# Kernel tuning notes

Measured on AMD Instinct MI355X. Metric: run time of the kernel, lower is better.

## Reference

```python
import jax, jax.numpy as jnp
import numpy as np


def setup_inputs() -> dict:
    key = jax.random.key(0)
    k1, k2 = jax.random.split(key)
    B, T, S, D = 8, 1024, 1024, 2048
    support_sets = jax.random.normal(k1, (B, S, D), dtype=jnp.float32)
    X_hats = jax.random.normal(k2, (B, T, D), dtype=jnp.float32)
    return {"support_sets": support_sets, "X_hats": X_hats}


def reference(support_sets, X_hats):
    # Pairwise cosine similarity: out[b, t, s] = cos(X_hats[b, t], support_sets[b, s])
    # Matches torch.nn.functional.cosine_similarity with eps=1e-10:
    #   dot / max(||x|| * ||y||, eps)
    eps = 1e-10
    x_norm = jnp.linalg.norm(X_hats, axis=-1)          # [B, T]
    s_norm = jnp.linalg.norm(support_sets, axis=-1)    # [B, S]
    dots = jnp.einsum('btd,bsd->bts', X_hats, support_sets)  # [B, T, S]
    denom = jnp.maximum(x_norm[:, :, None] * s_norm[:, None, :], eps)
    return dots / denom
```

## Files before the change

kernel.cpp:

```cpp
#include <hip/hip_runtime.h>
#include <hip/hip_bf16.h>

typedef __attribute__((ext_vector_type(4))) float        f32x4;
typedef __attribute__((ext_vector_type(8))) short        s16x8;
typedef __attribute__((ext_vector_type(4))) unsigned int u32x4;
typedef __attribute__((ext_vector_type(2))) unsigned int u32x2;

#define Bb 8
#define Tt 1024
#define Ss 1024
#define Dd 2048
#define BM 128
#define BN 128
#define BK 64

__device__ __forceinline__ unsigned pack2_bf16(float f0, float f1) {
  unsigned u0 = __builtin_bit_cast(unsigned, f0) + 0x8000u;
  unsigned u1 = __builtin_bit_cast(unsigned, f1) + 0x8000u;
  return (u0 >> 16) | (u1 & 0xffff0000u);
}

__device__ __forceinline__ void gld_lds16(const void* g, void* l) {
  __builtin_amdgcn_global_load_lds(
      (__attribute__((address_space(1))) void*)(void*)(g),
      (__attribute__((address_space(3))) void*)l, 16, 0, 0);
}

__global__ __launch_bounds__(256, 4)
void convert_kernel(const float* __restrict__ sup, const float* __restrict__ xh,
                    unsigned* __restrict__ abf, unsigned* __restrict__ bbf,
                    float* __restrict__ invA, float* __restrict__ invB)
{
  const int wave = threadIdx.x >> 6, lane = threadIdx.x & 63;
  const int rowg = (blockIdx.x * 4 + wave) * 2;
  const float* src; unsigned* dst; float* inv; int row;
  if (rowg < 8192) { row = rowg;         src = xh;  dst = abf; inv = invA; }
  else             { row = rowg - 8192;  src = sup; dst = bbf; inv = invB; }

  const f32x4* s0 = (const f32x4*)(src + (size_t)row * Dd);
  const f32x4* s1 = (const f32x4*)(src + (size_t)(row + 1) * Dd);
  u32x2* d0 = (u32x2*)(dst + (size_t)row * (Dd / 2));
  u32x2* d1 = (u32x2*)(dst + (size_t)(row + 1) * (Dd / 2));
  float sq0 = 0.0f, sq1 = 0.0f;
  #pragma unroll
  for (int j = 0; j < 8; ++j) {
    f32x4 v0 = s0[j * 64 + lane];
    f32x4 v1 = s1[j * 64 + lane];
    sq0 = fmaf(v0[0], v0[0], fmaf(v0[1], v0[1], fmaf(v0[2], v0[2], fmaf(v0[3], v0[3], sq0))));
    sq1 = fmaf(v1[0], v1[0], fmaf(v1[1], v1[1], fmaf(v1[2], v1[2], fmaf(v1[3], v1[3], sq1))));
    d0[j * 64 + lane] = (u32x2){pack2_bf16(v0[0], v0[1]), pack2_bf16(v0[2], v0[3])};
    d1[j * 64 + lane] = (u32x2){pack2_bf16(v1[0], v1[1]), pack2_bf16(v1[2], v1[3])};
  }
  #pragma unroll
  for (int m = 32; m; m >>= 1) { sq0 += __shfl_xor(sq0, m, 64); sq1 += __shfl_xor(sq1, m, 64); }
  if (lane == 0) { inv[row] = 1.0f / sqrtf(sq0); inv[row + 1] = 1.0f / sqrtf(sq1); }
}

__global__ __launch_bounds__(256, 2)
void gemm_kernel(const short* __restrict__ abf, const short* __restrict__ bbf,
                 const float* __restrict__ invA, const float* __restrict__ invB,
                 float* __restrict__ out)
{
  __shared__ short As[BM * BK];
  __shared__ short Bs[BN * BK];

  const int bid  = blockIdx.x;
  const int b    = bid >> 6;
  const int tile = bid & 63;
  const int tm   = tile >> 3;
  const int tn   = tile & 7;

  const int t = threadIdx.x, wave = t >> 6, lane = t & 63;

  const int srow = lane >> 3;
  const int cph  = lane & 7;
  const int r0   = wave * 32;

  const size_t aRow = (size_t)(b * Tt + tm * BM);
  const size_t bRow = (size_t)(b * Ss + tn * BN);
  const short *gA0, *gA1, *gA2, *gA3, *gB0, *gB1, *gB2, *gB3;
  {
    int r;
    r = r0 + 0 * 8 + srow; gA0 = abf + (aRow + r) * Dd + (cph ^ (r & 7)) * 8;
                           gB0 = bbf + (bRow + r) * Dd + (cph ^ (r & 7)) * 8;
    r = r0 + 1 * 8 + srow; gA1 = abf + (aRow + r) * Dd + (cph ^ (r & 7)) * 8;
                           gB1 = bbf + (bRow + r) * Dd + (cph ^ (r & 7)) * 8;
    r = r0 + 2 * 8 + srow; gA2 = abf + (aRow + r) * Dd + (cph ^ (r & 7)) * 8;
                           gB2 = bbf + (bRow + r) * Dd + (cph ^ (r & 7)) * 8;
    r = r0 + 3 * 8 + srow; gA3 = abf + (aRow + r) * Dd + (cph ^ (r & 7)) * 8;
                           gB3 = bbf + (bRow + r) * Dd + (cph ^ (r & 7)) * 8;
  }
  short* lA0 = As + (r0 + 0)  * BK;
  short* lA1 = As + (r0 + 8)  * BK;
  short* lA2 = As + (r0 + 16) * BK;
  short* lA3 = As + (r0 + 24) * BK;
  short* lB0 = Bs + (r0 + 0)  * BK;
  short* lB1 = Bs + (r0 + 8)  * BK;
  short* lB2 = Bs + (r0 + 16) * BK;
  short* lB3 = Bs + (r0 + 24) * BK;

  const int wm = (wave >> 1) << 6;
  const int wn = (wave & 1) << 6;
  const int lm = lane & 15;
  const int kq = lane >> 4;

  f32x4 acc[4][4];
  #pragma unroll
  for (int i = 0; i < 4; ++i)
    #pragma unroll
    for (int j = 0; j < 4; ++j)
      acc[i][j] = (f32x4)0.0f;

  for (int k0 = 0; k0 < Dd; k0 += BK) {
    __syncthreads();
    gld_lds16(gA0, lA0); gld_lds16(gA1, lA1); gld_lds16(gA2, lA2); gld_lds16(gA3, lA3);
    gld_lds16(gB0, lB0); gld_lds16(gB1, lB1); gld_lds16(gB2, lB2); gld_lds16(gB3, lB3);
    gA0 += BK; gA1 += BK; gA2 += BK; gA3 += BK;
    gB0 += BK; gB1 += BK; gB2 += BK; gB3 += BK;
    __syncthreads();

    #pragma unroll
    for (int ks = 0; ks < 2; ++ks) {
      const int pchunk = ((ks * 4 + kq) ^ (lm & 7)) * 8;
      s16x8 af[4], bfr[4];
      #pragma unroll
      for (int i = 0; i < 4; ++i) {
        af[i]  = *(const s16x8*)(As + (wm + i * 16 + lm) * BK + pchunk);
        bfr[i] = *(const s16x8*)(Bs + (wn + i * 16 + lm) * BK + pchunk);
      }
      #pragma unroll
      for (int mi = 0; mi < 4; ++mi)
        #pragma unroll
        for (int ni = 0; ni < 4; ++ni)
          acc[mi][ni] = __builtin_amdgcn_mfma_f32_16x16x32_bf16(af[mi], bfr[ni], acc[mi][ni], 0, 0, 0);
    }
  }

  const float* iA = invA + b * Tt + tm * BM;
  const float* iB = invB + b * Ss + tn * BN;
  float* outb = out + (size_t)(b * Tt + tm * BM) * Ss + tn * BN;
  const int m0 = wm + kq * 4;
  const int n0 = wn + lm;
  #pragma unroll
  for (int mi = 0; mi < 4; ++mi) {
    #pragma unroll
    for (int r = 0; r < 4; ++r) {
      const int mrow = m0 + mi * 16 + r;
      const float ia = iA[mrow];
      float* orow = outb + (size_t)mrow * Ss;
      #pragma unroll
      for (int ni = 0; ni < 4; ++ni) {
        const int ncol = n0 + ni * 16;
        orow[ncol] = acc[mi][ni][r] * (ia * iB[ncol]);
      }
    }
  }
}

#define LDKF 40
#define BKF 32
__global__ __launch_bounds__(256, 2)
void paircos_kernel(const float* __restrict__ sup, const float* __restrict__ xh,
                    float* __restrict__ out)
{
  __shared__ short As[BM * LDKF];
  __shared__ short Bs[BN * LDKF];
  __shared__ float invA[BM];
  __shared__ float invB[BN];

  const int bid = blockIdx.x;
  const int b = bid >> 6, tile = bid & 63, tm = tile >> 3, tn = tile & 7;
  const float* Abase = xh  + (size_t)(b * Tt + tm * BM) * Dd;
  const float* Bbase = sup + (size_t)(b * Ss + tn * BN) * Dd;
  const int t = threadIdx.x, row = t >> 1, kh = t & 1;
  const f32x4* agp = (const f32x4*)(Abase + (size_t)row * Dd + kh * 16);
  const f32x4* bgp = (const f32x4*)(Bbase + (size_t)row * Dd + kh * 16);
  u32x4* awr = (u32x4*)(As + row * LDKF + kh * 16);
  u32x4* bwr = (u32x4*)(Bs + row * LDKF + kh * 16);
  const int wave = t >> 6, lane = t & 63;
  const int wm = (wave >> 1) << 6, wn = (wave & 1) << 6;
  const int lm = lane & 15, kq = lane >> 4;

  f32x4 acc[4][4];
  #pragma unroll
  for (int i = 0; i < 4; ++i)
    #pragma unroll
    for (int j = 0; j < 4; ++j) acc[i][j] = (f32x4)0.0f;
  float sqa = 0.0f, sqb = 0.0f;
  f32x4 areg[4], breg[4];
  #pragma unroll
  for (int i = 0; i < 4; ++i) { areg[i] = agp[i]; breg[i] = bgp[i]; }

  for (int k0 = 0; k0 < Dd; k0 += BKF) {
    unsigned pa[8], pb[8];
    #pragma unroll
    for (int i = 0; i < 4; ++i) {
      sqa = fmaf(areg[i][0], areg[i][0], sqa); sqa = fmaf(areg[i][1], areg[i][1], sqa);
      sqa = fmaf(areg[i][2], areg[i][2], sqa); sqa = fmaf(areg[i][3], areg[i][3], sqa);
      pa[i*2+0] = pack2_bf16(areg[i][0], areg[i][1]); pa[i*2+1] = pack2_bf16(areg[i][2], areg[i][3]);
      sqb = fmaf(breg[i][0], breg[i][0], sqb); sqb = fmaf(breg[i][1], breg[i][1], sqb);
      sqb = fmaf(breg[i][2], breg[i][2], sqb); sqb = fmaf(breg[i][3], breg[i][3], sqb);
      pb[i*2+0] = pack2_bf16(breg[i][0], breg[i][1]); pb[i*2+1] = pack2_bf16(breg[i][2], breg[i][3]);
    }
    __syncthreads();
    awr[0] = (u32x4){pa[0],pa[1],pa[2],pa[3]}; awr[1] = (u32x4){pa[4],pa[5],pa[6],pa[7]};
    bwr[0] = (u32x4){pb[0],pb[1],pb[2],pb[3]}; bwr[1] = (u32x4){pb[4],pb[5],pb[6],pb[7]};
    __syncthreads();
    if (k0 + BKF < Dd) {
      const int off = (k0 + BKF) >> 2;
      #pragma unroll
      for (int i = 0; i < 4; ++i) { areg[i] = agp[off + i]; breg[i] = bgp[off + i]; }
    }
    s16x8 af[4], bfr[4];
    #pragma unroll
    for (int i = 0; i < 4; ++i) {
      af[i]  = *(const s16x8*)(As + (wm + i*16 + lm) * LDKF + kq * 8);
      bfr[i] = *(const s16x8*)(Bs + (wn + i*16 + lm) * LDKF + kq * 8);
    }
    #pragma unroll
    for (int mi = 0; mi < 4; ++mi)
      #pragma unroll
      for (int ni = 0; ni < 4; ++ni)
        acc[mi][ni] = __builtin_amdgcn_mfma_f32_16x16x32_bf16(af[mi], bfr[ni], acc[mi][ni], 0, 0, 0);
  }
  __syncthreads();
  ((float*)As)[t] = sqa; ((float*)Bs)[t] = sqb;
  __syncthreads();
  if (t < 128) {
    invA[t] = 1.0f / sqrtf(((float*)As)[2*t] + ((float*)As)[2*t+1]);
    invB[t] = 1.0f / sqrtf(((float*)Bs)[2*t] + ((float*)Bs)[2*t+1]);
  }
  __syncthreads();
  float* outb = out + (size_t)(b * Tt + tm * BM) * Ss + tn * BN;
  const int m0 = wm + kq * 4, n0 = wn + lm;
  #pragma unroll
  for (int mi = 0; mi < 4; ++mi) {
    #pragma unroll
    for (int r = 0; r < 4; ++r) {
      const int mrow = m0 + mi * 16 + r;
      const float ia = invA[mrow];
      float* orow = outb + (size_t)mrow * Ss;
      #pragma unroll
      for (int ni = 0; ni < 4; ++ni) {
        const int ncol = n0 + ni * 16;
        orow[ncol] = acc[mi][ni][r] * (ia * invB[ncol]);
      }
    }
  }
}

extern "C" void kernel_launch(void* const* d_in, const int* in_sizes, int n_in,
                              void* d_out, int out_size, void* d_ws, size_t ws_size,
                              hipStream_t stream) {
  const float* sup = (const float*)d_in[0];
  const float* xh  = (const float*)d_in[1];
  float* out = (float*)d_out;

  const size_t nElem = (size_t)Bb * Tt * Dd;
  const size_t bfBytes = nElem * sizeof(short);
  const size_t NEED = 2 * bfBytes + 2 * (size_t)Bb * Tt * sizeof(float);

  if (ws_size >= NEED) {
    unsigned* abf = (unsigned*)d_ws;
    unsigned* bbf = (unsigned*)((char*)d_ws + bfBytes);
    float* invA = (float*)((char*)d_ws + 2 * bfBytes);
    float* invB = invA + (size_t)Bb * Tt;
    convert_kernel<<<dim3(2048), dim3(256), 0, stream>>>(sup, xh, abf, bbf, invA, invB);
    gemm_kernel<<<dim3(512), dim3(256), 0, stream>>>((const short*)abf, (const short*)bbf,
                                                     invA, invB, out);
  } else {
    paircos_kernel<<<dim3(512), dim3(256), 0, stream>>>(sup, xh, out);
  }
}
```

Before: 203.3 us.

## Double-buffer LDS tiles in GEMM and batch loads in convert kernel

The GEMM main loop now keeps two LDS buffers for A and B tiles. It issues the global-to-LDS load for the next K tile before running MFMA work on the current one, so memory latency overlaps compute and there is one barrier per tile instead of two. The convert kernel now issues all eight vector loads per row before doing the conversions, which exposes more memory-level parallelism. The cost is double the LDS footprint (64KB per block), which may limit occupancy against the launch bound of 2 blocks, plus extra registers in the convert kernel.

```diff
diff --git a/kernel.cpp b/kernel.cpp
--- a/kernel.cpp
+++ b/kernel.cpp
@@ -39,18 +39,29 @@
 
   const f32x4* s0 = (const f32x4*)(src + (size_t)row * Dd);
   const f32x4* s1 = (const f32x4*)(src + (size_t)(row + 1) * Dd);
+
+  f32x4 v0[8], v1[8];
+  #pragma unroll
+  for (int j = 0; j < 8; ++j) v0[j] = s0[j * 64 + lane];
+  #pragma unroll
+  for (int j = 0; j < 8; ++j) v1[j] = s1[j * 64 + lane];
+
   u32x2* d0 = (u32x2*)(dst + (size_t)row * (Dd / 2));
   u32x2* d1 = (u32x2*)(dst + (size_t)(row + 1) * (Dd / 2));
   float sq0 = 0.0f, sq1 = 0.0f;
   #pragma unroll
   for (int j = 0; j < 8; ++j) {
-    f32x4 v0 = s0[j * 64 + lane];
-    f32x4 v1 = s1[j * 64 + lane];
-    sq0 = fmaf(v0[0], v0[0], fmaf(v0[1], v0[1], fmaf(v0[2], v0[2], fmaf(v0[3], v0[3], sq0))));
-    sq1 = fmaf(v1[0], v1[0], fmaf(v1[1], v1[1], fmaf(v1[2], v1[2], fmaf(v1[3], v1[3], sq1))));
-    d0[j * 64 + lane] = (u32x2){pack2_bf16(v0[0], v0[1]), pack2_bf16(v0[2], v0[3])};
-    d1[j * 64 + lane] = (u32x2){pack2_bf16(v1[0], v1[1]), pack2_bf16(v1[2], v1[3])};
-  }
+    f32x4 a = v0[j];
+    sq0 = fmaf(a[0], a[0], fmaf(a[1], a[1], fmaf(a[2], a[2], fmaf(a[3], a[3], sq0))));
+    d0[j * 64 + lane] = (u32x2){pack2_bf16(a[0], a[1]), pack2_bf16(a[2], a[3])};
+  }
+  #pragma unroll
+  for (int j = 0; j < 8; ++j) {
+    f32x4 a = v1[j];
+    sq1 = fmaf(a[0], a[0], fmaf(a[1], a[1], fmaf(a[2], a[2], fmaf(a[3], a[3], sq1))));
+    d1[j * 64 + lane] = (u32x2){pack2_bf16(a[0], a[1]), pack2_bf16(a[2], a[3])};
+  }
+
   #pragma unroll
   for (int m = 32; m; m >>= 1) { sq0 += __shfl_xor(sq0, m, 64); sq1 += __shfl_xor(sq1, m, 64); }
   if (lane == 0) { inv[row] = 1.0f / sqrtf(sq0); inv[row + 1] = 1.0f / sqrtf(sq1); }
@@ -61,8 +72,8 @@
                  const float* __restrict__ invA, const float* __restrict__ invB,
                  float* __restrict__ out)
 {
-  __shared__ short As[BM * BK];
-  __shared__ short Bs[BN * BK];
+  __shared__ short As[2][BM * BK];
+  __shared__ short Bs[2][BN * BK];
 
   const int bid  = blockIdx.x;
   const int b    = bid >> 6;
@@ -90,14 +101,6 @@
     r = r0 + 3 * 8 + srow; gA3 = abf + (aRow + r) * Dd + (cph ^ (r & 7)) * 8;
                            gB3 = bbf + (bRow + r) * Dd + (cph ^ (r & 7)) * 8;
   }
-  short* lA0 = As + (r0 + 0)  * BK;
-  short* lA1 = As + (r0 + 8)  * BK;
-  short* lA2 = As + (r0 + 16) * BK;
-  short* lA3 = As + (r0 + 24) * BK;
-  short* lB0 = Bs + (r0 + 0)  * BK;
-  short* lB1 = Bs + (r0 + 8)  * BK;
-  short* lB2 = Bs + (r0 + 16) * BK;
-  short* lB3 = Bs + (r0 + 24) * BK;
 
   const int wm = (wave >> 1) << 6;
   const int wn = (wave & 1) << 6;
@@ -111,30 +114,50 @@
     for (int j = 0; j < 4; ++j)
       acc[i][j] = (f32x4)0.0f;
 
-  for (int k0 = 0; k0 < Dd; k0 += BK) {
-    __syncthreads();
-    gld_lds16(gA0, lA0); gld_lds16(gA1, lA1); gld_lds16(gA2, lA2); gld_lds16(gA3, lA3);
-    gld_lds16(gB0, lB0); gld_lds16(gB1, lB1); gld_lds16(gB2, lB2); gld_lds16(gB3, lB3);
-    gA0 += BK; gA1 += BK; gA2 += BK; gA3 += BK;
-    gB0 += BK; gB1 += BK; gB2 += BK; gB3 += BK;
-    __syncthreads();
-
-    #pragma unroll
-    for (int ks = 0; ks < 2; ++ks) {
-      const int pchunk = ((ks * 4 + kq) ^ (lm & 7)) * 8;
-      s16x8 af[4], bfr[4];
-      #pragma unroll
-      for (int i = 0; i < 4; ++i) {
-        af[i]  = *(const s16x8*)(As + (wm + i * 16 + lm) * BK + pchunk);
-        bfr[i] = *(const s16x8*)(Bs + (wn + i * 16 + lm) * BK + pchunk);
-      }
-      #pragma unroll
-      for (int mi = 0; mi < 4; ++mi)
-        #pragma unroll
-        for (int ni = 0; ni < 4; ++ni)
-          acc[mi][ni] = __builtin_amdgcn_mfma_f32_16x16x32_bf16(af[mi], bfr[ni], acc[mi][ni], 0, 0, 0);
-    }
-  }
+#define STAGE(bi) do {                                                   \
+    gld_lds16(gA0, As[bi] + (r0 + 0)  * BK);                             \
+    gld_lds16(gA1, As[bi] + (r0 + 8)  * BK);                             \
+    gld_lds16(gA2, As[bi] + (r0 + 16) * BK);                             \
+    gld_lds16(gA3, As[bi] + (r0 + 24) * BK);                             \
+    gld_lds16(gB0, Bs[bi] + (r0 + 0)  * BK);                             \
+    gld_lds16(gB1, Bs[bi] + (r0 + 8)  * BK);                             \
+    gld_lds16(gB2, Bs[bi] + (r0 + 16) * BK);                             \
+    gld_lds16(gB3, Bs[bi] + (r0 + 24) * BK);                             \
+    gA0 += BK; gA1 += BK; gA2 += BK; gA3 += BK;                          \
+    gB0 += BK; gB1 += BK; gB2 += BK; gB3 += BK;                          \
+  } while (0)
+
+#define COMPUTE(bi) do {                                                 \
+    _Pragma("unroll")                                                    \
+    for (int ks = 0; ks < 2; ++ks) {                                     \
+      const int pchunk = ((ks * 4 + kq) ^ (lm & 7)) * 8;                 \
+      s16x8 af[4], bfr[4];                                               \
+      _Pragma("unroll")                                                  \
+      for (int i = 0; i < 4; ++i) {                                      \
+        af[i]  = *(const s16x8*)(As[bi] + (wm + i * 16 + lm) * BK + pchunk); \
+        bfr[i] = *(const s16x8*)(Bs[bi] + (wn + i * 16 + lm) * BK + pchunk); \
+      }                                                                  \
+      _Pragma("unroll")                                                  \
+      for (int mi = 0; mi < 4; ++mi)                                     \
+        _Pragma("unroll")                                                \
+        for (int ni = 0; ni < 4; ++ni)                                   \
+          acc[mi][ni] = __builtin_amdgcn_mfma_f32_16x16x32_bf16(af[mi], bfr[ni], acc[mi][ni], 0, 0, 0); \
+    }                                                                    \
+  } while (0)
+
+  STAGE(0);
+  __syncthreads();
+
+  for (int k0 = 0; k0 < Dd; k0 += 2 * BK) {
+    STAGE(1);
+    COMPUTE(0);
+    __syncthreads();
+    if (k0 + 2 * BK < Dd) STAGE(0);
+    COMPUTE(1);
+    __syncthreads();
+  }
+#undef STAGE
+#undef COMPUTE
 
   const float* iA = invA + b * Tt + tm * BM;
   const float* iB = invB + b * Ss + tn * BN;
```

After: 207.1 us. No clear change (+1.9%).
